# Performance work log

Measured on AMD Instinct MI355X. Metric: run time of the kernel, lower is better.

Reference implementation:

```python
import jax, jax.numpy as jnp
import numpy as np

# DenoiseTransform(h=10, template_window_size=7, search_window_size=21)
KS = 7                 # odd template window -> kernel_size (7, 7)
SIGMA_COLOR = 10.0     # float(h)
SIGMA_SPACE = 21.0     # float(search_window_size), same for y and x


def _gauss1d(ks, sigma):
    # kornia.get_gaussian_kernel1d: centered, normalized to sum 1
    x = jnp.arange(ks, dtype=jnp.float32) - ks // 2
    g = jnp.exp(-0.5 * (x / sigma) ** 2)
    return g / g.sum()


def setup_inputs() -> dict:
    key = jax.random.key(0)
    # batch of 8 RGB 512x512 images in [0, 1]
    img = jax.random.uniform(key, (8, 3, 512, 512), dtype=jnp.float32)
    return {"img": img}


def reference(img):
    """kornia.filters.bilateral_blur(img, (7,7), 10.0, (21.0,21.0)),
    border_type='reflect', color_distance_type='l1'.
    Fused over the 7x7 window: never materializes (B,C,H,W,49)."""
    ks = KS
    pad = ks // 2
    space = jnp.outer(_gauss1d(ks, SIGMA_SPACE), _gauss1d(ks, SIGMA_SPACE))  # (ks, ks)
    B, C, H, W = img.shape
    padded = jnp.pad(img, ((0, 0), (0, 0), (pad, pad), (pad, pad)), mode="reflect")
    num = jnp.zeros_like(img)                      # (B, C, H, W)
    den = jnp.zeros((B, 1, H, W), dtype=img.dtype)  # (B, 1, H, W)
    neg_half_inv_sc2 = -0.5 / (SIGMA_COLOR ** 2)
    for i in range(ks):          # fixed small 7x7 window -> static unrolled loop
        for j in range(ks):
            patch = jax.lax.dynamic_slice(padded, (0, 0, i, j), (B, C, H, W))
            # L1 color distance over channels, then squared (kornia default 'l1')
            d = jnp.abs(patch - img).sum(axis=1, keepdims=True)  # (B,1,H,W)
            w = space[i, j] * jnp.exp(neg_half_inv_sc2 * d * d)   # (B,1,H,W)
            num = num + w * patch
            den = den + w
    return num / den
```

## Files before the change

### kernel.cpp

```cpp
#include <hip/hip_runtime.h>

#define BB 8
#define HH 512
#define WW 512
#define HW (HH * WW)
#define STRIP 8

__device__ __forceinline__ int reflect512(int v) {
    v = v < 0 ? -v : v;
    return v >= 512 ? 1022 - v : v;
}

__global__ __launch_bounds__(256, 2) void bilateral_march(const float* __restrict__ in,
                                                          float* __restrict__ out) {
    const int blk   = blockIdx.x;
    const int b     = blk >> 7;
    const int rem   = blk & 127;
    const int strip = rem >> 1;
    const int xh    = rem & 1;
    const int x     = xh * 256 + threadIdx.x;
    const int ys    = strip * STRIP;

    const float* __restrict__ p0 = in + (size_t)b * 3 * HW;
    const float* __restrict__ p1 = p0 + HW;
    const float* __restrict__ p2 = p1 + HW;

    int colo[7];
    #pragma unroll
    for (int c = 0; c < 7; ++c) colo[c] = reflect512(x - 3 + c);

    float w0[7][7], w1[7][7], w2[7][7];
    #pragma unroll
    for (int j = 0; j < 7; ++j) {
        int rb = reflect512(ys - 3 + j) * WW;
        #pragma unroll
        for (int c = 0; c < 7; ++c) {
            int o = rb + colo[c];
            w0[j][c] = p0[o]; w1[j][c] = p1[o]; w2[j][c] = p2[o];
        }
    }

    const float ls7[7] = {-0.01472138f, -0.00654284f, -0.00163571f, 0.f,
                          -0.00163571f, -0.00654284f, -0.01472138f};
    const float K2 = -0.00721347520445f;

    #pragma unroll
    for (int k = 0; k < STRIP; ++k) {
        float t0[7], t1[7], t2[7];
        if (k < STRIP - 1) {
            int rb = reflect512(ys + k + 4) * WW;
            #pragma unroll
            for (int c = 0; c < 7; ++c) {
                int o = rb + colo[c];
                t0[c] = p0[o]; t1[c] = p1[o]; t2[c] = p2[o];
            }
        }

        const int cs = (k + 3) % 7;
        const float c0 = w0[cs][3], c1 = w1[cs][3], c2 = w2[cs][3];
        float n0 = 0.f, n1 = 0.f, n2 = 0.f, dn = 0.f;

        #pragma unroll
        for (int j = 0; j < 7; ++j) {
            const int s = (k + j) % 7;
            #pragma unroll
            for (int c = 0; c < 7; ++c) {
                float a0 = w0[s][c], a1 = w1[s][c], a2 = w2[s][c];
                float d  = fabsf(a0 - c0) + fabsf(a1 - c1) + fabsf(a2 - c2);
                float wt = __builtin_amdgcn_exp2f(fmaf(K2, d * d, ls7[j] + ls7[c]));
                n0 += wt * a0; n1 += wt * a1; n2 += wt * a2; dn += wt;
            }
        }

        const float inv = 1.0f / dn;
        size_t ob = (size_t)b * 3 * HW + (size_t)(ys + k) * WW + x;
        out[ob]          = n0 * inv;
        out[ob + HW]     = n1 * inv;
        out[ob + 2 * HW] = n2 * inv;

        if (k < STRIP - 1) {
            const int ns = k % 7;
            #pragma unroll
            for (int c = 0; c < 7; ++c) {
                w0[ns][c] = t0[c]; w1[ns][c] = t1[c]; w2[ns][c] = t2[c];
            }
        }
    }
}

extern "C" void kernel_launch(void* const* d_in, const int* in_sizes, int n_in,
                              void* d_out, int out_size, void* d_ws, size_t ws_size,
                              hipStream_t stream) {
    const float* in = (const float*)d_in[0];
    float* out = (float*)d_out;
    int blocks = BB * (WW / 256) * (HH / STRIP);
    bilateral_march<<<blocks, 256, 0, stream>>>(in, out);
}
```

Before: 46.48 us.

## Compute bilateral weights and accumulation in packed half2 arithmetic

```diff
diff --git a/kernel.cpp b/kernel.cpp
--- a/kernel.cpp
+++ b/kernel.cpp
@@ -1,4 +1,5 @@
 #include <hip/hip_runtime.h>
+#include <hip/hip_fp16.h>
 
 #define BB 8
 #define HH 512
@@ -11,8 +12,8 @@
     return v >= 512 ? 1022 - v : v;
 }
 
-__global__ __launch_bounds__(256, 2) void bilateral_march(const float* __restrict__ in,
-                                                          float* __restrict__ out) {
+__global__ __launch_bounds__(256, 2) void bilateral_h2(const float* __restrict__ in,
+                                                       float* __restrict__ out) {
     const int blk   = blockIdx.x;
     const int b     = blk >> 7;
     const int rem   = blk & 127;
@@ -25,52 +26,81 @@
     const float* __restrict__ p1 = p0 + HW;
     const float* __restrict__ p2 = p1 + HW;
 
-    int colo[7];
+    int colo[8];
     #pragma unroll
-    for (int c = 0; c < 7; ++c) colo[c] = reflect512(x - 3 + c);
+    for (int c = 0; c < 8; ++c) colo[c] = reflect512(x - 3 + c);
 
-    float w0[7][7], w1[7][7], w2[7][7];
+    const float ls7[7] = {-0.01472138f, -0.00654284f, -0.00163571f, 0.f,
+                          -0.00163571f, -0.00654284f, -0.01472138f};
+    const float lsx[8] = {-0.01472138f, -0.00654284f, -0.00163571f, 0.f,
+                          -0.00163571f, -0.00654284f, -0.01472138f, -1000.0f};
+    const __half2 k2 = __float2half2_rn(-0.00721347520445f);
+
+    __half2 w0[7][4], w1[7][4], w2[7][4];
     #pragma unroll
     for (int j = 0; j < 7; ++j) {
         int rb = reflect512(ys - 3 + j) * WW;
         #pragma unroll
-        for (int c = 0; c < 7; ++c) {
-            int o = rb + colo[c];
-            w0[j][c] = p0[o]; w1[j][c] = p1[o]; w2[j][c] = p2[o];
+        for (int i = 0; i < 4; ++i) {
+            int oa = rb + colo[2 * i], ob = rb + colo[2 * i + 1];
+            w0[j][i] = __floats2half2_rn(p0[oa], p0[ob]);
+            w1[j][i] = __floats2half2_rn(p1[oa], p1[ob]);
+            w2[j][i] = __floats2half2_rn(p2[oa], p2[ob]);
         }
     }
 
-    const float ls7[7] = {-0.01472138f, -0.00654284f, -0.00163571f, 0.f,
-                          -0.00163571f, -0.00654284f, -0.01472138f};
-    const float K2 = -0.00721347520445f;
-
     #pragma unroll
     for (int k = 0; k < STRIP; ++k) {
-        float t0[7], t1[7], t2[7];
+        __half2 t0[4], t1[4], t2[4];
         if (k < STRIP - 1) {
             int rb = reflect512(ys + k + 4) * WW;
             #pragma unroll
-            for (int c = 0; c < 7; ++c) {
-                int o = rb + colo[c];
-                t0[c] = p0[o]; t1[c] = p1[o]; t2[c] = p2[o];
+            for (int i = 0; i < 4; ++i) {
+                int oa = rb + colo[2 * i], ob = rb + colo[2 * i + 1];
+                t0[i] = __floats2half2_rn(p0[oa], p0[ob]);
+                t1[i] = __floats2half2_rn(p1[oa], p1[ob]);
+                t2[i] = __floats2half2_rn(p2[oa], p2[ob]);
             }
         }
 
         const int cs = (k + 3) % 7;
-        const float c0 = w0[cs][3], c1 = w1[cs][3], c2 = w2[cs][3];
-        float n0 = 0.f, n1 = 0.f, n2 = 0.f, dn = 0.f;
+        const __half2 c0 = __high2half2(w0[cs][1]);
+        const __half2 c1 = __high2half2(w1[cs][1]);
+        const __half2 c2 = __high2half2(w2[cs][1]);
+
+        __half2 a0[2] = {__float2half2_rn(0.f), __float2half2_rn(0.f)};
+        __half2 a1[2] = {__float2half2_rn(0.f), __float2half2_rn(0.f)};
+        __half2 a2[2] = {__float2half2_rn(0.f), __float2half2_rn(0.f)};
+        __half2 ad[2] = {__float2half2_rn(0.f), __float2half2_rn(0.f)};
 
         #pragma unroll
         for (int j = 0; j < 7; ++j) {
             const int s = (k + j) % 7;
+            const int h = j & 1;
             #pragma unroll
-            for (int c = 0; c < 7; ++c) {
-                float a0 = w0[s][c], a1 = w1[s][c], a2 = w2[s][c];
-                float d  = fabsf(a0 - c0) + fabsf(a1 - c1) + fabsf(a2 - c2);
-                float wt = __builtin_amdgcn_exp2f(fmaf(K2, d * d, ls7[j] + ls7[c]));
-                n0 += wt * a0; n1 += wt * a1; n2 += wt * a2; dn += wt;
+            for (int i = 0; i < 4; ++i) {
+                const __half2 lw = __floats2half2_rn(ls7[j] + lsx[2 * i],
+                                                     ls7[j] + lsx[2 * i + 1]);
+                __half2 q0 = w0[s][i], q1 = w1[s][i], q2 = w2[s][i];
+                __half2 d  = __habs2(__hsub2(q0, c0));
+                d = __hadd2(d, __habs2(__hsub2(q1, c1)));
+                d = __hadd2(d, __habs2(__hsub2(q2, c2)));
+                __half2 wt = h2exp2(__hfma2(k2, __hmul2(d, d), lw));
+                a0[h] = __hfma2(wt, q0, a0[h]);
+                a1[h] = __hfma2(wt, q1, a1[h]);
+                a2[h] = __hfma2(wt, q2, a2[h]);
+                ad[h] = __hadd2(ad[h], wt);
             }
         }
+
+        float2 f0a = __half22float2(a0[0]), f0b = __half22float2(a0[1]);
+        float2 f1a = __half22float2(a1[0]), f1b = __half22float2(a1[1]);
+        float2 f2a = __half22float2(a2[0]), f2b = __half22float2(a2[1]);
+        float2 fda = __half22float2(ad[0]), fdb = __half22float2(ad[1]);
+        float n0 = f0a.x + f0a.y + f0b.x + f0b.y;
+        float n1 = f1a.x + f1a.y + f1b.x + f1b.y;
+        float n2 = f2a.x + f2a.y + f2b.x + f2b.y;
+        float dn = fda.x + fda.y + fdb.x + fdb.y;
 
         const float inv = 1.0f / dn;
         size_t ob = (size_t)b * 3 * HW + (size_t)(ys + k) * WW + x;
@@ -81,8 +111,8 @@
         if (k < STRIP - 1) {
             const int ns = k % 7;
             #pragma unroll
-            for (int c = 0; c < 7; ++c) {
-                w0[ns][c] = t0[c]; w1[ns][c] = t1[c]; w2[ns][c] = t2[c];
+            for (int i = 0; i < 4; ++i) {
+                w0[ns][i] = t0[i]; w1[ns][i] = t1[i]; w2[ns][i] = t2[i];
             }
         }
     }
@@ -94,5 +124,5 @@
     const float* in = (const float*)d_in[0];
     float* out = (float*)d_out;
     int blocks = BB * (WW / 256) * (HH / STRIP);
-    bilateral_march<<<blocks, 256, 0, stream>>>(in, out);
+    bilateral_h2<<<blocks, 256, 0, stream>>>(in, out);
 }
```

Result: slower. 50.11 us (+7.8%).
